# Kernel optimization log

Hardware: AMD Instinct MI355X
Metric: run time of the kernel (lower is better)

The kernel has to match this reference:

```python
import jax, jax.numpy as jnp
import numpy as np

N, D, H, C, K = 16384, 128, 128, 10, 32  # cells, in-dim, hidden, classes, kNN neighbors


def setup_inputs() -> dict:
    key = jax.random.key(0)
    k0, k1, k2 = jax.random.split(key, 3)
    return {
        "X": jax.random.normal(k0, (N, D), dtype=jnp.float32),
        "W1": jax.random.normal(k1, (2 * D, H), dtype=jnp.float32) * 0.05,
        "b1": jnp.zeros((H,), dtype=jnp.float32),
        "W2": jax.random.normal(k2, (2 * H, C), dtype=jnp.float32) * 0.05,
        "b2": jnp.zeros((C,), dtype=jnp.float32),
    }


def _knn_idx(X, k):
    # knn_graph(X, k, loop=True): k nearest neighbors incl. self per node
    sq = jnp.sum(X * X, axis=1)
    d2 = sq[:, None] - 2.0 * (X @ X.T) + sq[None, :]  # [N, N] squared dists
    _, idx = jax.lax.top_k(-d2, k)  # [N, k] neighbor indices (self has d2=0)
    return idx


def _edge_conv(X, idx, W, b, relu):
    # PyG EdgeConv: out_i = max_j mlp(concat(x_i, x_j - x_i))
    xi = X[:, None, :]                 # [N, 1, d]
    xj = X[idx]                        # [N, k, d] gather
    msg = jnp.concatenate([jnp.broadcast_to(xi, xj.shape), xj - xi], axis=-1)
    h = msg @ W + b                    # [N, k, out]
    if relu:
        h = jax.nn.relu(h)
    return jnp.max(h, axis=1)          # max aggregation over neighbors


def reference(X, W1, b1, W2, b2):
    # dropout p=0.0 -> identity
    idx = _knn_idx(X, K)               # graph built once, reused (edge_index cached)
    h = _edge_conv(X, idx, W1, b1, relu=True)
    out = _edge_conv(h, idx, W2, b2, relu=False)
    return out
```

## Files before the change

kernel.cpp:

```cpp
#include <hip/hip_runtime.h>
#include <math.h>

#define Nn 16384
#define Dd 128
#define Kk 32
#define JSPLIT 8
#define JCH (Nn / JSPLIT)
#define NG (JCH / 16)
#define CAP 48
#define MAXSLOT 3
#define BAND 0.4f
#define ZQ 2.4176f

typedef unsigned short u16;
typedef short short8 __attribute__((ext_vector_type(8)));
typedef float f32x4 __attribute__((ext_vector_type(4)));

__device__ __forceinline__ u16 f2bf(float x) {
    unsigned u = __float_as_uint(x);
    unsigned r = u + 0x7FFFu + ((u >> 16) & 1u);
    return (u16)(r >> 16);
}

__global__ __launch_bounds__(256) void prep_kernel(const float* __restrict__ X,
                                                   u16* __restrict__ Xhi,
                                                   float* __restrict__ sqn,
                                                   float* __restrict__ thrA,
                                                   int* __restrict__ flagCnt) {
    const int i = blockIdx.x * 4 + (threadIdx.x >> 6);
    const int lane = threadIdx.x & 63;
    const float2 v = *(const float2*)(X + (size_t)i * Dd + lane * 2);
    const unsigned pack = ((unsigned)f2bf(v.y) << 16) | (unsigned)f2bf(v.x);
    *(unsigned*)(Xhi + (size_t)i * Dd + lane * 2) = pack;
    float s = fmaf(v.x, v.x, v.y * v.y);
#pragma unroll
    for (int o = 32; o > 0; o >>= 1) s += __shfl_down(s, o);
    if (lane == 0) {
        sqn[i] = s;
        thrA[i] = 128.0f - ZQ * sqrtf(256.0f + 4.0f * s);
    }
    if (blockIdx.x == 0 && threadIdx.x == 0) *flagCnt = 0;
}

__global__ __launch_bounds__(256, 2) void knn_filter(const u16* __restrict__ Xhi,
                                                     const float* __restrict__ sqn,
                                                     const float* __restrict__ thrA,
                                                     u16* __restrict__ cand,
                                                     int* __restrict__ candCnt) {
    __shared__ u16 listS[256][CAP];
    __shared__ int cntS[256];

    const int tid = threadIdx.x;
    const int wave = tid >> 6, lane = tid & 63;
    const int quad = lane >> 4, n16 = lane & 15;
    const int itile = blockIdx.x >> 3, chunk = blockIdx.x & 7;
    const int ibase = itile * 256;
    const int wbase = ibase + wave * 64;
    const int jch0 = chunk * JCH;

    short8 aF[4][4];
#pragma unroll
    for (int is = 0; is < 4; is++) {
        const u16* arow = Xhi + (size_t)(wbase + is * 16 + n16) * Dd + quad * 8;
#pragma unroll
        for (int ks = 0; ks < 4; ks++) aF[is][ks] = *(const short8*)(arow + ks * 32);
    }
    float nhT[16];
    int cntReg[16];
#pragma unroll
    for (int is = 0; is < 4; is++)
#pragma unroll
        for (int r = 0; r < 4; r++) {
            nhT[is * 4 + r] = -0.5f * thrA[wbase + is * 16 + quad * 4 + r];
            cntReg[is * 4 + r] = 0;
        }

    const u16* bbase = Xhi + (size_t)(jch0 + n16) * Dd + quad * 8;
    short8 bb[2][4];
    float sj[2];
#pragma unroll
    for (int ks = 0; ks < 4; ks++) bb[0][ks] = *(const short8*)(bbase + ks * 32);
    sj[0] = sqn[jch0 + n16];
#pragma unroll
    for (int ks = 0; ks < 4; ks++) bb[1][ks] = *(const short8*)(bbase + 16 * Dd + ks * 32);
    sj[1] = sqn[jch0 + 16 + n16];

#define PROC(p, gg)                                                            \
    {                                                                          \
        const float bias = -0.5f * sj[p];                                      \
        f32x4 acc[4];                                                          \
        acc[0] = (f32x4){bias, bias, bias, bias};                              \
        acc[1] = acc[0]; acc[2] = acc[0]; acc[3] = acc[0];                     \
        _Pragma("unroll")                                                      \
        for (int ks = 0; ks < 4; ks++) {                                       \
            acc[0] = __builtin_amdgcn_mfma_f32_16x16x32_bf16(aF[0][ks], bb[p][ks], acc[0], 0, 0, 0); \
            acc[1] = __builtin_amdgcn_mfma_f32_16x16x32_bf16(aF[1][ks], bb[p][ks], acc[1], 0, 0, 0); \
            acc[2] = __builtin_amdgcn_mfma_f32_16x16x32_bf16(aF[2][ks], bb[p][ks], acc[2], 0, 0, 0); \
            acc[3] = __builtin_amdgcn_mfma_f32_16x16x32_bf16(aF[3][ks], bb[p][ks], acc[3], 0, 0, 0); \
        }                                                                      \
        {      \
            const u16* nb = bbase + (size_t)((gg) + 2) * 16 * Dd;              \
            bb[p][0] = *(const short8*)(nb);                                   \
            bb[p][1] = *(const short8*)(nb + 32);                              \
            bb[p][2] = *(const short8*)(nb + 64);                              \
            bb[p][3] = *(const short8*)(nb + 96);                              \
            sj[p] = sqn[jch0 + ((gg) + 2) * 16 + n16];                         \
        }                                                                      \
        const int jj = jch0 + (gg) * 16 + n16;                                 \
        _Pragma("unroll")                                                      \
        for (int is = 0; is < 4; is++) {                                       \
            _Pragma("unroll")                                                  \
            for (int r = 0; r < 4; r++) {                                      \
                const unsigned long long mr = __ballot(acc[is][r] > nhT[is * 4 + r]); \
                if (mr) {    \
                    const unsigned qm = (unsigned)((mr >> (quad * 16)) & 0xFFFFull); \
                    if ((qm >> n16) & 1u) {                                    \
                        const int pos = cntReg[is * 4 + r] + __popc(qm & ((1u << n16) - 1u)); \
                        if (pos < CAP)                                         \
                            listS[wave * 64 + is * 16 + quad * 4 + r][pos] = (u16)jj; \
                    }                                                          \
                    cntReg[is * 4 + r] += __popc(qm);                          \
                }                                                              \
            }                                                                  \
        }                                                                      \
    }

    for (int g = 0; g < NG; g += 2) {
        PROC(0, g)
        PROC(1, g + 1)
    }
#undef PROC

    if (n16 == 0) {
#pragma unroll
        for (int is = 0; is < 4; is++)
#pragma unroll
            for (int r = 0; r < 4; r++)
                cntS[wave * 64 + is * 16 + quad * 4 + r] = cntReg[is * 4 + r];
    }
    for (int rl = 0; rl < 64; rl++) {
        const int row = wave * 64 + rl;
        const int n = cntS[row];
        const int gi = ibase + row;
        if (lane == 0) candCnt[(size_t)gi * JSPLIT + chunk] = n;
        if (lane < min(n, CAP))
            cand[((size_t)gi * JSPLIT + chunk) * CAP + lane] = listS[row][lane];
    }
}

__global__ __launch_bounds__(256) void knn_exact(const float* __restrict__ X,
                                                 const float* __restrict__ sqn,
                                                 const float* __restrict__ thrA,
                                                 const u16* __restrict__ cand,
                                                 const int* __restrict__ candCnt,
                                                 int* __restrict__ idx_out,
                                                 int* __restrict__ flagCnt,
                                                 int* __restrict__ flagRows) {
    const int wave = threadIdx.x >> 6, lane = threadIdx.x & 63;
    const int quad = lane >> 4, n16 = lane & 15;
    const int i = blockIdx.x * 4 + wave;

    float4 xi[8];
    {
        const float4* xb = (const float4*)(X + (size_t)i * Dd + quad * 32);
#pragma unroll
        for (int u = 0; u < 8; u++) xi[u] = xb[u];
    }
    int pre[JSPLIT];
    bool over = false;
    int M = 0;
#pragma unroll
    for (int k = 0; k < JSPLIT; k++) {
        int c = candCnt[(size_t)i * JSPLIT + k];
        over = over || (c > CAP);
        pre[k] = M;
        M += min(c, CAP);
    }
    over = over || (M > 64 * MAXSLOT);
    if (over) {
        if (lane == 0) { const int f = atomicAdd(flagCnt, 1); flagRows[f] = i; }
        return;
    }
    const float rvT = thrA[i];

    float rv[MAXSLOT];
    int jd[MAXSLOT];
#pragma unroll
    for (int s = 0; s < MAXSLOT; s++) { rv[s] = INFINITY; jd[s] = -1; }

#pragma unroll
    for (int s = 0; s < MAXSLOT; s++) {
#pragma unroll
        for (int t = 0; t < 4; t++) {
            const int c = s * 64 + t * 16 + n16;
            if (c < M) {
                int k = 0;
#pragma unroll
                for (int q = 1; q < JSPLIT; q++) if (c >= pre[q]) k = q;
                const int jj = cand[((size_t)i * JSPLIT + k) * CAP + (c - pre[k])];
                const float4* xb = (const float4*)(X + (size_t)jj * Dd + quad * 32);
                float s0 = 0.f, s1 = 0.f, s2 = 0.f, s3 = 0.f;
#pragma unroll
                for (int u = 0; u < 8; u++) {
                    const float4 b = xb[u];
                    s0 = fmaf(xi[u].x, b.x, s0); s1 = fmaf(xi[u].y, b.y, s1);
                    s2 = fmaf(xi[u].z, b.z, s2); s3 = fmaf(xi[u].w, b.w, s3);
                }
                float p = (s0 + s1) + (s2 + s3);
                p += __shfl_xor(p, 16);
                p += __shfl_xor(p, 32);
                if (quad == t) { rv[s] = fmaf(-2.f, p, sqn[jj]); jd[s] = jj; }
            }
        }
    }

    int good = 0;
#pragma unroll
    for (int s = 0; s < MAXSLOT; s++) good += __popcll(__ballot(rv[s] < rvT - BAND));
    if (good < Kk) {
        if (lane == 0) { const int f = atomicAdd(flagCnt, 1); flagRows[f] = i; }
        return;
    }
    int rk[MAXSLOT] = {0, 0, 0};
    for (int s2 = 0; s2 < 64; s2++) {
        float ov[MAXSLOT];
#pragma unroll
        for (int s = 0; s < MAXSLOT; s++) ov[s] = __shfl(rv[s], s2);
#pragma unroll
        for (int s = 0; s < MAXSLOT; s++) {
            const int myid = lane + 64 * s;
#pragma unroll
            for (int t = 0; t < MAXSLOT; t++)
                rk[s] += (ov[t] < rv[s] || (ov[t] == rv[s] && s2 + 64 * t < myid)) ? 1 : 0;
        }
    }
#pragma unroll
    for (int s = 0; s < MAXSLOT; s++)
        if (jd[s] >= 0 && rk[s] < Kk) idx_out[(size_t)i * Kk + rk[s]] = jd[s];
}

__global__ __launch_bounds__(256) void knn_cleanup(const float* __restrict__ X,
                                                   const float* __restrict__ sqn,
                                                   const int* __restrict__ flagCnt,
                                                   const int* __restrict__ flagRows,
                                                   float* __restrict__ scratch,
                                                   int* __restrict__ idx_out) {
    __shared__ float xi[Dd];
    __shared__ int cntS;
    __shared__ float lv[256];
    __shared__ int lj[256];
    const int tid = threadIdx.x;
    const int lane = tid & 63;
    const int F = *flagCnt;
    float* rvS = scratch + (size_t)blockIdx.x * Nn;
    for (int f = blockIdx.x; f < F; f += gridDim.x) {
        const int i = flagRows[f];
        __syncthreads();
        if (tid < Dd) xi[tid] = X[(size_t)i * Dd + tid];
        __syncthreads();
        for (int j = tid; j < Nn; j += 256) {
            const float* xj = X + (size_t)j * Dd;
            float s0 = 0.f, s1 = 0.f, s2 = 0.f, s3 = 0.f;
#pragma unroll
            for (int d = 0; d < Dd; d += 4) {
                const float4 a = *(const float4*)&xi[d];
                const float4 b = *(const float4*)(xj + d);
                s0 = fmaf(a.x, b.x, s0); s1 = fmaf(a.y, b.y, s1);
                s2 = fmaf(a.z, b.z, s2); s3 = fmaf(a.w, b.w, s3);
            }
            rvS[j] = fmaf(-2.f, (s0 + s1) + (s2 + s3), sqn[j]);
        }
        __syncthreads();
        float lo = -1.0e9f, hi = 1.0e9f, T = 1.0e9f;
        for (int it = 0; it < 48; it++) {
            const float mid = 0.5f * (lo + hi);
            int local = 0;
            for (int j = tid; j < Nn; j += 256) local += (rvS[j] < mid) ? 1 : 0;
#pragma unroll
            for (int o = 32; o > 0; o >>= 1) local += __shfl_down(local, o);
            __syncthreads();
            if (tid == 0) cntS = 0;
            __syncthreads();
            if (lane == 0) atomicAdd(&cntS, local);
            __syncthreads();
            const int c = cntS;
            if (c < Kk) lo = mid;
            else if (c > 200) hi = mid;
            else { T = mid; break; }
        }
        if (T == 1.0e9f) T = hi;
        __syncthreads();
        if (tid == 0) cntS = 0;
        __syncthreads();
        for (int j = tid; j < Nn; j += 256) {
            if (rvS[j] < T) {
                const int p = atomicAdd(&cntS, 1);
                if (p < 256) { lv[p] = rvS[j]; lj[p] = j; }
            }
        }
        __syncthreads();
        const int n = min(cntS, 256);
        if (tid < 64) {
            float v[4]; int jjj[4]; int rk2[4] = {0, 0, 0, 0};
#pragma unroll
            for (int s = 0; s < 4; s++) {
                const int sl = lane + 64 * s;
                v[s] = (sl < n) ? lv[sl] : INFINITY;
                jjj[s] = (sl < n) ? lj[sl] : -1;
            }
            for (int s2 = 0; s2 < 64; s2++) {
                const float o0 = __shfl(v[0], s2), o1 = __shfl(v[1], s2);
                const float o2 = __shfl(v[2], s2), o3 = __shfl(v[3], s2);
#pragma unroll
                for (int s = 0; s < 4; s++) {
                    const int myid = lane + 64 * s;
                    rk2[s] += (o0 < v[s] || (o0 == v[s] && s2 < myid));
                    rk2[s] += (o1 < v[s] || (o1 == v[s] && s2 + 64 < myid));
                    rk2[s] += (o2 < v[s] || (o2 == v[s] && s2 + 128 < myid));
                    rk2[s] += (o3 < v[s] || (o3 == v[s] && s2 + 192 < myid));
                }
            }
#pragma unroll
            for (int s = 0; s < 4; s++)
                if (jjj[s] >= 0 && rk2[s] < Kk) idx_out[(size_t)i * Kk + rk2[s]] = jjj[s];
        }
        __syncthreads();
    }
}

__global__ __launch_bounds__(256) void pq_kernel(const float* __restrict__ X,
                                                 const float* __restrict__ W1,
                                                 const float* __restrict__ b1,
                                                 float* __restrict__ P,
                                                 float* __restrict__ Q) {
    __shared__ float xrow[16][Dd];
    const int i0 = blockIdx.x * 16;
    for (int t = threadIdx.x; t < 16 * Dd / 4; t += 256)
        ((float4*)&xrow[0][0])[t] = ((const float4*)(X + (size_t)i0 * Dd))[t];
    __syncthreads();
    const int cc = threadIdx.x & 127;
    const int mat = threadIdx.x >> 7;
    float acc[16];
#pragma unroll
    for (int r = 0; r < 16; r++) acc[r] = 0.f;
    for (int d = 0; d < Dd; d++) {
        float w;
        if (mat == 0) w = W1[d * 128 + cc] - W1[(128 + d) * 128 + cc];
        else          w = W1[(128 + d) * 128 + cc];
#pragma unroll
        for (int r = 0; r < 16; r++) acc[r] = fmaf(xrow[r][d], w, acc[r]);
    }
    if (mat == 0) {
        const float b = b1[cc];
#pragma unroll
        for (int r = 0; r < 16; r++) P[(size_t)(i0 + r) * 128 + cc] = acc[r] + b;
    } else {
#pragma unroll
        for (int r = 0; r < 16; r++) Q[(size_t)(i0 + r) * 128 + cc] = acc[r];
    }
}

__global__ __launch_bounds__(128) void h1_kernel(const float* __restrict__ P,
                                                 const float* __restrict__ Q,
                                                 const int* __restrict__ idx,
                                                 float* __restrict__ h1) {
    const int i = blockIdx.x;
    const int c = threadIdx.x;
    __shared__ int jb[Kk];
    if (threadIdx.x < Kk) jb[threadIdx.x] = idx[(size_t)i * Kk + threadIdx.x];
    __syncthreads();
    float m = -INFINITY;
#pragma unroll
    for (int k = 0; k < Kk; k++) m = fmaxf(m, Q[(size_t)jb[k] * 128 + c]);
    h1[(size_t)i * 128 + c] = fmaxf(P[(size_t)i * 128 + c] + m, 0.f);
}

__global__ __launch_bounds__(256) void pq2_kernel(const float* __restrict__ h1,
                                                  const float* __restrict__ W2,
                                                  const float* __restrict__ b2,
                                                  float* __restrict__ P2,
                                                  float* __restrict__ Q2) {
    __shared__ float w2s[2560];
    __shared__ float h1s[16][132];
    const int i0 = blockIdx.x * 16;
    for (int t = threadIdx.x; t < 640; t += 256)
        ((float4*)w2s)[t] = ((const float4*)W2)[t];
    {
        const int r = threadIdx.x >> 4, q = (threadIdx.x & 15) * 8;
        *(float4*)&h1s[r][q]     = *(const float4*)(h1 + (size_t)(i0 + r) * 128 + q);
        *(float4*)&h1s[r][q + 4] = *(const float4*)(h1 + (size_t)(i0 + r) * 128 + q + 4);
    }
    __syncthreads();
    const int il = threadIdx.x >> 4, c = threadIdx.x & 15;
    if (c >= 10) return;
    float pa = 0.f, pb = 0.f;
#pragma unroll 4
    for (int d = 0; d < Dd; d++) {
        const float h = h1s[il][d];
        const float wa = w2s[d * 10 + c];
        const float wb = w2s[(128 + d) * 10 + c];
        pa = fmaf(h, wa - wb, pa);
        pb = fmaf(h, wb, pb);
    }
    P2[(size_t)(i0 + il) * 10 + c] = pa + b2[c];
    Q2[(size_t)(i0 + il) * 10 + c] = pb;
}

__global__ __launch_bounds__(256) void out_kernel(const float* __restrict__ P2,
                                                  const float* __restrict__ Q2,
                                                  const int* __restrict__ idx,
                                                  float* __restrict__ out) {
    const int g = blockIdx.x * 256 + threadIdx.x;
    const int i = g >> 4;
    const int c = g & 15;
    if (c >= 10) return;
    const int* jr = idx + (size_t)i * Kk;
    float m = -INFINITY;
#pragma unroll
    for (int k = 0; k < Kk; k++) m = fmaxf(m, Q2[(size_t)jr[k] * 10 + c]);
    out[(size_t)i * 10 + c] = P2[(size_t)i * 10 + c] + m;
}

extern "C" void kernel_launch(void* const* d_in, const int* in_sizes, int n_in,
                              void* d_out, int out_size, void* d_ws, size_t ws_size,
                              hipStream_t stream) {
    const float* X  = (const float*)d_in[0];
    const float* W1 = (const float*)d_in[1];
    const float* b1 = (const float*)d_in[2];
    const float* W2 = (const float*)d_in[3];
    const float* b2 = (const float*)d_in[4];
    float* out = (float*)d_out;

    char* ws = (char*)d_ws;
    float* sqn     = (float*)(ws + 0);
    float* thrA    = (float*)(ws + 73728);
    int*   flagCnt = (int*)(ws + 139264);
    int*   flagRows= (int*)(ws + 139392);
    int*   idx     = (int*)(ws + 262144);
    u16*   Xhi     = (u16*)(ws + 2359296);
    float* P       = (float*)(ws + 6561792);
    float* Q       = P + (size_t)Nn * 128;
    float* h1      = Q + (size_t)Nn * 128;
    float* P2      = h1 + (size_t)Nn * 128;
    float* Q2      = P2 + (size_t)Nn * 10;
    u16* cand    = (u16*)P;
    int* candCnt = (int*)((char*)P + 13631488);
    float* cleanupScratch = P;

    prep_kernel<<<Nn / 4, 256, 0, stream>>>(X, Xhi, sqn, thrA, flagCnt);
    knn_filter<<<64 * JSPLIT, 256, 0, stream>>>(Xhi, sqn, thrA, cand, candCnt);
    knn_exact<<<Nn / 4, 256, 0, stream>>>(X, sqn, thrA, cand, candCnt, idx, flagCnt, flagRows);
    knn_cleanup<<<256, 256, 0, stream>>>(X, sqn, flagCnt, flagRows, cleanupScratch, idx);
    pq_kernel<<<Nn / 16, 256, 0, stream>>>(X, W1, b1, P, Q);
    h1_kernel<<<Nn, 128, 0, stream>>>(P, Q, idx, h1);
    pq2_kernel<<<Nn / 16, 256, 0, stream>>>(h1, W2, b2, P2, Q2);
    out_kernel<<<Nn * 16 / 256, 256, 0, stream>>>(P2, Q2, idx, out);
}
```

Baseline: 406.6 us.

## Software-pipeline MFMA distance tiles with ballot threshold filtering

```diff
diff --git a/kernel.cpp b/kernel.cpp
--- a/kernel.cpp
+++ b/kernel.cpp
@@ -85,18 +85,17 @@
     for (int ks = 0; ks < 4; ks++) bb[1][ks] = *(const short8*)(bbase + 16 * Dd + ks * 32);
     sj[1] = sqn[jch0 + 16 + n16];
 
-#define PROC(p, gg)                                                            \
+#define MSTEP(p, gg)                                                           \
     {                                                                          \
         const float bias = -0.5f * sj[p];                                      \
-        f32x4 acc[4];                                                          \
-        acc[0] = (f32x4){bias, bias, bias, bias};                              \
-        acc[1] = acc[0]; acc[2] = acc[0]; acc[3] = acc[0];                     \
+        acc##p[0] = (f32x4){bias, bias, bias, bias};                           \
+        acc##p[1] = acc##p[0]; acc##p[2] = acc##p[0]; acc##p[3] = acc##p[0];   \
         _Pragma("unroll")                                                      \
         for (int ks = 0; ks < 4; ks++) {                                       \
-            acc[0] = __builtin_amdgcn_mfma_f32_16x16x32_bf16(aF[0][ks], bb[p][ks], acc[0], 0, 0, 0); \
-            acc[1] = __builtin_amdgcn_mfma_f32_16x16x32_bf16(aF[1][ks], bb[p][ks], acc[1], 0, 0, 0); \
-            acc[2] = __builtin_amdgcn_mfma_f32_16x16x32_bf16(aF[2][ks], bb[p][ks], acc[2], 0, 0, 0); \
-            acc[3] = __builtin_amdgcn_mfma_f32_16x16x32_bf16(aF[3][ks], bb[p][ks], acc[3], 0, 0, 0); \
+            acc##p[0] = __builtin_amdgcn_mfma_f32_16x16x32_bf16(aF[0][ks], bb[p][ks], acc##p[0], 0, 0, 0); \
+            acc##p[1] = __builtin_amdgcn_mfma_f32_16x16x32_bf16(aF[1][ks], bb[p][ks], acc##p[1], 0, 0, 0); \
+            acc##p[2] = __builtin_amdgcn_mfma_f32_16x16x32_bf16(aF[2][ks], bb[p][ks], acc##p[2], 0, 0, 0); \
+            acc##p[3] = __builtin_amdgcn_mfma_f32_16x16x32_bf16(aF[3][ks], bb[p][ks], acc##p[3], 0, 0, 0); \
         }                                                                      \
         {      \
             const u16* nb = bbase + (size_t)((gg) + 2) * 16 * Dd;              \
@@ -106,12 +105,16 @@
             bb[p][3] = *(const short8*)(nb + 96);                              \
             sj[p] = sqn[jch0 + ((gg) + 2) * 16 + n16];                         \
         }                                                                      \
+    }
+
+#define TSTEP(p, gg)                                                           \
+    {                                                                          \
         const int jj = jch0 + (gg) * 16 + n16;                                 \
         _Pragma("unroll")                                                      \
         for (int is = 0; is < 4; is++) {                                       \
             _Pragma("unroll")                                                  \
             for (int r = 0; r < 4; r++) {                                      \
-                const unsigned long long mr = __ballot(acc[is][r] > nhT[is * 4 + r]); \
+                const unsigned long long mr = __ballot(acc##p[is][r] > nhT[is * 4 + r]); \
                 if (mr) {    \
                     const unsigned qm = (unsigned)((mr >> (quad * 16)) & 0xFFFFull); \
                     if ((qm >> n16) & 1u) {                                    \
@@ -125,11 +128,19 @@
         }                                                                      \
     }
 
-    for (int g = 0; g < NG; g += 2) {
-        PROC(0, g)
-        PROC(1, g + 1)
-    }
-#undef PROC
+    f32x4 acc0[4], acc1[4];
+    MSTEP(0, 0)
+    for (int g = 0; g < NG - 2; g += 2) {
+        MSTEP(1, g + 1)
+        TSTEP(0, g)
+        MSTEP(0, g + 2)
+        TSTEP(1, g + 1)
+    }
+    MSTEP(1, NG - 1)
+    TSTEP(0, NG - 2)
+    TSTEP(1, NG - 1)
+#undef MSTEP
+#undef TSTEP
 
     if (n16 == 0) {
 #pragma unroll
```

Measured after the change: 407.6 us. About the same (+0.2%).

## Deepen kNN filter prefetch, make candidate append branchless, shrink candidate capacity

Applied to the files above, without the earlier changes.

```diff
diff --git a/kernel.cpp b/kernel.cpp
--- a/kernel.cpp
+++ b/kernel.cpp
@@ -7,8 +7,8 @@
 #define JSPLIT 8
 #define JCH (Nn / JSPLIT)
 #define NG (JCH / 16)
-#define CAP 48
-#define MAXSLOT 3
+#define CAP 32
+#define MAXSLOT 2
 #define BAND 0.4f
 #define ZQ 2.4176f
 
@@ -47,7 +47,7 @@
                                                      const float* __restrict__ thrA,
                                                      u16* __restrict__ cand,
                                                      int* __restrict__ candCnt) {
-    __shared__ u16 listS[256][CAP];
+    __shared__ u16 listF[256 * CAP + 256];
     __shared__ int cntS[256];
 
     const int tid = threadIdx.x;
@@ -57,6 +57,8 @@
     const int ibase = itile * 256;
     const int wbase = ibase + wave * 64;
     const int jch0 = chunk * JCH;
+    const unsigned below = (1u << n16) - 1u;
+    const int scrapOff = 256 * CAP + tid;
 
     short8 aF[4][4];
 #pragma unroll
@@ -76,14 +78,15 @@
         }
 
     const u16* bbase = Xhi + (size_t)(jch0 + n16) * Dd + quad * 8;
-    short8 bb[2][4];
-    float sj[2];
-#pragma unroll
-    for (int ks = 0; ks < 4; ks++) bb[0][ks] = *(const short8*)(bbase + ks * 32);
-    sj[0] = sqn[jch0 + n16];
-#pragma unroll
-    for (int ks = 0; ks < 4; ks++) bb[1][ks] = *(const short8*)(bbase + 16 * Dd + ks * 32);
-    sj[1] = sqn[jch0 + 16 + n16];
+    short8 bb[4][4];
+    float sj[4];
+#pragma unroll
+    for (int p = 0; p < 4; p++) {
+        const u16* pb = bbase + (size_t)p * 16 * Dd;
+#pragma unroll
+        for (int ks = 0; ks < 4; ks++) bb[p][ks] = *(const short8*)(pb + ks * 32);
+        sj[p] = sqn[jch0 + p * 16 + n16];
+    }
 
 #define PROC(p, gg)                                                            \
     {                                                                          \
@@ -98,36 +101,39 @@
             acc[2] = __builtin_amdgcn_mfma_f32_16x16x32_bf16(aF[2][ks], bb[p][ks], acc[2], 0, 0, 0); \
             acc[3] = __builtin_amdgcn_mfma_f32_16x16x32_bf16(aF[3][ks], bb[p][ks], acc[3], 0, 0, 0); \
         }                                                                      \
-        {      \
-            const u16* nb = bbase + (size_t)((gg) + 2) * 16 * Dd;              \
+        {    \
+            const int gp = ((gg) + 4) & (NG - 1);                              \
+            const u16* nb = bbase + (size_t)gp * 16 * Dd;                      \
             bb[p][0] = *(const short8*)(nb);                                   \
             bb[p][1] = *(const short8*)(nb + 32);                              \
             bb[p][2] = *(const short8*)(nb + 64);                              \
             bb[p][3] = *(const short8*)(nb + 96);                              \
-            sj[p] = sqn[jch0 + ((gg) + 2) * 16 + n16];                         \
+            sj[p] = sqn[jch0 + gp * 16 + n16];                                 \
         }                                                                      \
         const int jj = jch0 + (gg) * 16 + n16;                                 \
         _Pragma("unroll")                                                      \
         for (int is = 0; is < 4; is++) {                                       \
             _Pragma("unroll")                                                  \
             for (int r = 0; r < 4; r++) {                                      \
-                const unsigned long long mr = __ballot(acc[is][r] > nhT[is * 4 + r]); \
-                if (mr) {    \
-                    const unsigned qm = (unsigned)((mr >> (quad * 16)) & 0xFFFFull); \
-                    if ((qm >> n16) & 1u) {                                    \
-                        const int pos = cntReg[is * 4 + r] + __popc(qm & ((1u << n16) - 1u)); \
-                        if (pos < CAP)                                         \
-                            listS[wave * 64 + is * 16 + quad * 4 + r][pos] = (u16)jj; \
-                    }                                                          \
-                    cntReg[is * 4 + r] += __popc(qm);                          \
-                }                                                              \
+                const int ir = is * 4 + r;                                     \
+                const bool h = acc[is][r] > nhT[ir];                           \
+                const unsigned long long mr = __ballot(h);                     \
+                const unsigned qm = (unsigned)(mr >> (quad * 16)) & 0xFFFFu;   \
+                const int pos = cntReg[ir] + __popc(qm & below);               \
+                const bool wr = h && (pos < CAP);                              \
+                const int rowbase = (wave * 64 + is * 16 + quad * 4 + r) * CAP; \
+                const int off = wr ? rowbase + pos : scrapOff;                 \
+                listF[off] = (u16)jj;        \
+                cntReg[ir] += __popc(qm);                                      \
             }                                                                  \
         }                                                                      \
     }
 
-    for (int g = 0; g < NG; g += 2) {
+    for (int g = 0; g < NG; g += 4) {
         PROC(0, g)
         PROC(1, g + 1)
+        PROC(2, g + 2)
+        PROC(3, g + 3)
     }
 #undef PROC
 
@@ -144,7 +150,7 @@
         const int gi = ibase + row;
         if (lane == 0) candCnt[(size_t)gi * JSPLIT + chunk] = n;
         if (lane < min(n, CAP))
-            cand[((size_t)gi * JSPLIT + chunk) * CAP + lane] = listS[row][lane];
+            cand[((size_t)gi * JSPLIT + chunk) * CAP + lane] = listF[row * CAP + lane];
     }
 }
 
@@ -221,7 +227,7 @@
         if (lane == 0) { const int f = atomicAdd(flagCnt, 1); flagRows[f] = i; }
         return;
     }
-    int rk[MAXSLOT] = {0, 0, 0};
+    int rk[MAXSLOT] = {};
     for (int s2 = 0; s2 < 64; s2++) {
         float ov[MAXSLOT];
 #pragma unroll
```

New measurement: 444.4 us. 1.09x slower.
